# Performance work log

Measured on AMD Instinct MI355X. Metric: run time of the kernel, lower is better.

The kernel has to match this reference:

```python
import jax, jax.numpy as jnp
import numpy as np

B, S, D, H = 4, 1024, 1024, 16
HD = D // H  # head dim = 64


def setup_inputs() -> dict:
    key = jax.random.key(0)
    ks = jax.random.split(key, 12)
    inv = 1.0 / np.sqrt(D)
    inp = {
        "q": jax.random.normal(ks[0], (B, S, D), jnp.float32),
        "k": jax.random.normal(ks[1], (B, S, D), jnp.float32),
        "v": jax.random.normal(ks[2], (B, S, D), jnp.float32),
        # additive-style mask: 1 where attention is disallowed (causal)
        "mask": jnp.triu(jnp.ones((S, S), jnp.float32), k=1)[None, None, :, :],
        "Wq": jax.random.normal(ks[3], (D, D), jnp.float32) * inv,
        "bq": jnp.zeros((D,), jnp.float32),
        "Wk": jax.random.normal(ks[4], (D, D), jnp.float32) * inv,
        "bk": jnp.zeros((D,), jnp.float32),
        "Wv": jax.random.normal(ks[5], (D, D), jnp.float32) * inv,
        "bv": jnp.zeros((D,), jnp.float32),
        "Wo": jax.random.normal(ks[6], (D, D), jnp.float32) * inv,
        "bo": jnp.zeros((D,), jnp.float32),
    }
    return inp


def _split_heads(x):
    # [b, s, (h d)] -> [b, h, s, d]
    b, s, _ = x.shape
    return x.reshape(b, s, H, HD).transpose(0, 2, 1, 3)


def reference(q, k, v, mask, Wq, bq, Wk, bk, Wv, bv, Wo, bo):
    query = _split_heads(q @ Wq + bq)   # [b,h,s,d]
    key = _split_heads(k @ Wk + bk)
    value = _split_heads(v @ Wv + bv)

    scores = jnp.einsum("bhqd,bhkd->bhqk", query, key) / np.sqrt(HD)
    scores = scores + mask * (-1e12)
    attention_weights = jax.nn.softmax(scores, axis=-1)  # [b,h,s,s]
    attn = jnp.einsum("bhqk,bhkd->bhqd", attention_weights, value)

    # dropout is identity in eval mode
    attn = attn.transpose(0, 2, 1, 3).reshape(q.shape[0], q.shape[1], D)
    out = attn @ Wo + bo
    return out, attention_weights
```

## Files before the change

kernel.cpp:

```cpp
#include <hip/hip_runtime.h>
#include <hip/hip_bf16.h>

#define B_ 4
#define S_ 1024
#define D_ 1024
#define H_ 16
#define HD_ 64
#define M_ (B_*S_)
#define NT_ (S_/64)

typedef __attribute__((ext_vector_type(8))) short bf16x8;
typedef __attribute__((ext_vector_type(8))) unsigned short u16x8;
typedef __attribute__((ext_vector_type(4))) float f32x4;

typedef __attribute__((address_space(1))) const unsigned int g_uint;
typedef __attribute__((address_space(3))) unsigned int l_uint;

__device__ __forceinline__ unsigned short f2bf(float f) {
  unsigned int x = __builtin_bit_cast(unsigned int, f);
  unsigned int r = (x + 0x7fffu + ((x >> 16) & 1u)) >> 16;
  return (unsigned short)r;
}
__device__ __forceinline__ float bf2f(unsigned short u) {
  unsigned int x = ((unsigned int)u) << 16;
  return __builtin_bit_cast(float, x);
}
__device__ __forceinline__ void load_lds16(const ushort* g, ushort* l) {
  __builtin_amdgcn_global_load_lds((g_uint*)g, (l_uint*)l, 16, 0, 0);
}

__global__ void cvt3(const float* __restrict__ q, const float* __restrict__ k,
                     const float* __restrict__ v, ushort* __restrict__ qo,
                     ushort* __restrict__ ko, ushort* __restrict__ vo) {
  const float* s; ushort* d;
  switch (blockIdx.y) {
    case 0: s = q; d = qo; break;
    case 1: s = k; d = ko; break;
    default: s = v; d = vo; break;
  }
  int n4 = (M_ * D_) / 4;
  for (int i = blockIdx.x * blockDim.x + threadIdx.x; i < n4; i += gridDim.x * blockDim.x) {
    float4 x = reinterpret_cast<const float4*>(s)[i];
    ushort4 o;
    o.x = f2bf(x.x); o.y = f2bf(x.y); o.z = f2bf(x.z); o.w = f2bf(x.w);
    reinterpret_cast<ushort4*>(d)[i] = o;
  }
}

__global__ void tr4(const float* __restrict__ Wq, const float* __restrict__ Wk,
                    const float* __restrict__ Wv, const float* __restrict__ Wo,
                    ushort* __restrict__ q, ushort* __restrict__ k,
                    ushort* __restrict__ v, ushort* __restrict__ o) {
  const float* W; ushort* WT;
  switch (blockIdx.z) {
    case 0: W = Wq; WT = q; break;
    case 1: W = Wk; WT = k; break;
    case 2: W = Wv; WT = v; break;
    default: W = Wo; WT = o; break;
  }
  __shared__ float tile[32][33];
  int tx = threadIdx.x & 31, ty = threadIdx.x >> 5;
  int bx = blockIdx.x * 32, by = blockIdx.y * 32;
  for (int r = 0; r < 32; r += 8)
    tile[ty + r][tx] = W[(size_t)(by + ty + r) * D_ + bx + tx];
  __syncthreads();
  for (int r = 0; r < 32; r += 8)
    WT[(size_t)(bx + ty + r) * D_ + by + tx] = f2bf(tile[tx][ty + r]);
}

template <int BF16OUT>
__device__ __forceinline__ void gemm_body(const ushort* __restrict__ A,
                                          const ushort* __restrict__ Bt,
                                          const float* __restrict__ bias,
                                          void* __restrict__ Cp,
                                          int bm, int bn, int N, int K) {
  __shared__ ushort Al[128 * 64];
  __shared__ ushort Bl[64 * 64];
  const int tid = threadIdx.x;
  const int wave = tid >> 6, lane = tid & 63;
  const int r0 = lane & 15, kq = lane >> 4;
  const int wr = wave >> 1, wc = wave & 1;
  const int sl = lane >> 3;
  const int sc8 = ((lane & 7) ^ (lane >> 3)) * 8;
  f32x4 zero = {0.f, 0.f, 0.f, 0.f};
  f32x4 acc[4][2];
#pragma unroll
  for (int m = 0; m < 4; ++m)
    for (int n = 0; n < 2; ++n) acc[m][n] = zero;

  for (int kt = 0; kt < K; kt += 64) {
    __syncthreads();
#pragma unroll
    for (int i = 0; i < 6; ++i) {
      int c = wave * 6 + i;
      if (c < 16) {
        load_lds16(A + (size_t)(bm + c * 8 + sl) * K + kt + sc8, &Al[c * 512]);
      } else {
        int cb = c - 16;
        load_lds16(Bt + (size_t)(bn + cb * 8 + sl) * K + kt + sc8, &Bl[cb * 512]);
      }
    }
    __syncthreads();
#pragma unroll
    for (int kk = 0; kk < 2; ++kk) {
      bf16x8 a[4], b[2];
#pragma unroll
      for (int m = 0; m < 4; ++m) {
        int row = wr * 64 + m * 16 + r0;
        a[m] = *(const bf16x8*)&Al[row * 64 + (((kk * 4 + kq) ^ (r0 & 7)) * 8)];
      }
#pragma unroll
      for (int n = 0; n < 2; ++n) {
        int row = wc * 32 + n * 16 + r0;
        b[n] = *(const bf16x8*)&Bl[row * 64 + (((kk * 4 + kq) ^ (r0 & 7)) * 8)];
      }
#pragma unroll
      for (int m = 0; m < 4; ++m)
#pragma unroll
        for (int n = 0; n < 2; ++n)
          acc[m][n] = __builtin_amdgcn_mfma_f32_16x16x32_bf16(a[m], b[n], acc[m][n], 0, 0, 0);
    }
  }

#pragma unroll
  for (int m = 0; m < 4; ++m) {
#pragma unroll
    for (int n = 0; n < 2; ++n) {
      int col = bn + wc * 32 + n * 16 + r0;
      float bv = bias[col];
#pragma unroll
      for (int j = 0; j < 4; ++j) {
        int row = bm + wr * 64 + m * 16 + kq * 4 + j;
        float v = acc[m][n][j] + bv;
        if (BF16OUT) ((ushort*)Cp)[(size_t)row * N + col] = f2bf(v);
        else         ((float*)Cp)[(size_t)row * N + col] = v;
      }
    }
  }
}

__global__ __launch_bounds__(256) void gemm_qkv(const ushort* __restrict__ qa,
                                                const ushort* __restrict__ ka,
                                                const ushort* __restrict__ va,
                                                const ushort* __restrict__ WqT,
                                                const ushort* __restrict__ WkT,
                                                const ushort* __restrict__ WvT,
                                                const float* __restrict__ bq,
                                                const float* __restrict__ bk,
                                                const float* __restrict__ bv,
                                                ushort* __restrict__ Qo,
                                                ushort* __restrict__ Ko,
                                                ushort* __restrict__ Vo) {
  const ushort* A; const ushort* Bt; const float* bias; ushort* C;
  switch (blockIdx.z) {
    case 0: A = qa; Bt = WqT; bias = bq; C = Qo; break;
    case 1: A = ka; Bt = WkT; bias = bk; C = Ko; break;
    default: A = va; Bt = WvT; bias = bv; C = Vo; break;
  }
  gemm_body<1>(A, Bt, bias, C, blockIdx.x * 128, blockIdx.y * 64, D_, D_);
}

__global__ __launch_bounds__(256) void gemm_out(const ushort* __restrict__ A,
                                                const ushort* __restrict__ Bt,
                                                const float* __restrict__ bias,
                                                float* __restrict__ C) {
  gemm_body<0>(A, Bt, bias, C, blockIdx.x * 128, blockIdx.y * 64, D_, D_);
}

__global__ __launch_bounds__(256) void attn_fused(const ushort* __restrict__ Qb,
                                                  const ushort* __restrict__ Kb,
                                                  const ushort* __restrict__ Vb,
                                                  float* __restrict__ wout,
                                                  ushort* __restrict__ ctx) {
  const int h = blockIdx.y, b = blockIdx.z;
  const int tid = threadIdx.x, wave = tid >> 6, lane = tid & 63;
  const int r0 = lane & 15, kq = lane >> 4;
  const int sl = lane >> 3;
  const int sc8 = ((lane & 7) ^ (lane >> 3)) * 8;
  __shared__ ushort Qt[64 * 64];
  __shared__ ushort Kt[64 * 64];
  __shared__ ushort Vt[64 * 64];
  __shared__ ushort Wl[4][16 * 64];
  __shared__ float rs_lds[4][16];
  float* wbase = wout + (size_t)((b * H_ + h) * S_) * S_;

  for (int pp = 0; pp < 2; ++pp) {
    const int qt = pp ? (NT_ - 1 - blockIdx.x) : blockIdx.x;
    __syncthreads();
    {
      const ushort* Qg = Qb + ((size_t)(b * S_ + qt * 64)) * D_ + h * 64;
#pragma unroll
      for (int i = 0; i < 2; ++i) {
        int c = wave * 2 + i;
        load_lds16(Qg + (size_t)(c * 8 + sl) * D_ + sc8, &Qt[c * 512]);
      }
    }
    __syncthreads();
    bf16x8 qa0, qa1;
    {
      int row = wave * 16 + r0;
      qa0 = *(const bf16x8*)&Qt[row * 64 + ((kq ^ (r0 & 7)) * 8)];
      qa1 = *(const bf16x8*)&Qt[row * 64 + (((4 + kq) ^ (r0 & 7)) * 8)];
    }
    const int grow0 = qt * 64 + wave * 16 + kq * 4;

    float partial[4] = {0.f, 0.f, 0.f, 0.f};
    for (int vb = 0; vb <= qt; ++vb) {
      __syncthreads();
      const ushort* Kg = Kb + ((size_t)(b * S_ + vb * 64)) * D_ + h * 64;
#pragma unroll
      for (int i = 0; i < 2; ++i) {
        int c = wave * 2 + i;
        load_lds16(Kg + (size_t)(c * 8 + sl) * D_ + sc8, &Kt[c * 512]);
      }
      __syncthreads();
      const bool diag = (vb == qt);
#pragma unroll
      for (int jt = 0; jt < 4; ++jt) {
        int krow = jt * 16 + r0;
        bf16x8 kb0 = *(const bf16x8*)&Kt[krow * 64 + ((kq ^ (r0 & 7)) * 8)];
        bf16x8 kb1 = *(const bf16x8*)&Kt[krow * 64 + (((4 + kq) ^ (r0 & 7)) * 8)];
        f32x4 sc = {0.f, 0.f, 0.f, 0.f};
        sc = __builtin_amdgcn_mfma_f32_16x16x32_bf16(qa0, kb0, sc, 0, 0, 0);
        sc = __builtin_amdgcn_mfma_f32_16x16x32_bf16(qa1, kb1, sc, 0, 0, 0);
        int col = vb * 64 + krow;
#pragma unroll
        for (int j = 0; j < 4; ++j) {
          float e = (diag && col > grow0 + j) ? 0.f : __expf(sc[j] * 0.125f);
          partial[j] += e;
        }
      }
    }
    float rs[4];
#pragma unroll
    for (int j = 0; j < 4; ++j) {
      float s = partial[j];
#pragma unroll
      for (int off = 1; off < 16; off <<= 1) s += __shfl_xor(s, off, 64);
      rs[j] = 1.f / s;
    }
    if (r0 == 0) {
#pragma unroll
      for (int j = 0; j < 4; ++j) rs_lds[wave][kq * 4 + j] = rs[j];
    }

    f32x4 zero = {0.f, 0.f, 0.f, 0.f};
    f32x4 cacc[4];
#pragma unroll
    for (int nt = 0; nt < 4; ++nt) cacc[nt] = zero;

    for (int vb = 0; vb <= qt; ++vb) {
      __syncthreads();
      const ushort* Kg = Kb + ((size_t)(b * S_ + vb * 64)) * D_ + h * 64;
      const ushort* Vg = Vb + ((size_t)(b * S_ + vb * 64)) * D_ + h * 64;
#pragma unroll
      for (int i = 0; i < 2; ++i) {
        int c = wave * 2 + i;
        load_lds16(Kg + (size_t)(c * 8 + sl) * D_ + sc8, &Kt[c * 512]);
      }
#pragma unroll
      for (int it = 0; it < 2; ++it) {
        int seg = wave * 2 + it;
        ushort tmp[8];
        *(uint4*)tmp = *(const uint4*)&Vg[(size_t)lane * D_ + seg * 8];
#pragma unroll
        for (int e = 0; e < 8; ++e) Vt[(seg * 8 + e) * 64 + (lane ^ (e << 3))] = tmp[e];
      }
      __syncthreads();
      const bool diag = (vb == qt);
#pragma unroll
      for (int jt = 0; jt < 4; ++jt) {
        int krow = jt * 16 + r0;
        bf16x8 kb0 = *(const bf16x8*)&Kt[krow * 64 + ((kq ^ (r0 & 7)) * 8)];
        bf16x8 kb1 = *(const bf16x8*)&Kt[krow * 64 + (((4 + kq) ^ (r0 & 7)) * 8)];
        f32x4 sc = {0.f, 0.f, 0.f, 0.f};
        sc = __builtin_amdgcn_mfma_f32_16x16x32_bf16(qa0, kb0, sc, 0, 0, 0);
        sc = __builtin_amdgcn_mfma_f32_16x16x32_bf16(qa1, kb1, sc, 0, 0, 0);
        int col = vb * 64 + krow;
#pragma unroll
        for (int j = 0; j < 4; ++j) {
          int rowW = kq * 4 + j;
          float e = (diag && col > grow0 + j) ? 0.f : __expf(sc[j] * 0.125f);
          Wl[wave][rowW * 64 + ((jt * 16 + r0) ^ ((rowW & 7) << 3))] = f2bf(e);
        }
      }
#pragma unroll
      for (int ks = 0; ks < 2; ++ks) {
        bf16x8 af = *(const bf16x8*)&Wl[wave][r0 * 64 + (((ks * 4 + kq) ^ (r0 & 7)) * 8)];
#pragma unroll
        for (int nt = 0; nt < 4; ++nt) {
          bf16x8 vf = *(const bf16x8*)&Vt[(nt * 16 + r0) * 64 + (((ks * 4 + kq) ^ (r0 & 7)) * 8)];
          cacc[nt] = __builtin_amdgcn_mfma_f32_16x16x32_bf16(af, vf, cacc[nt], 0, 0, 0);
        }
      }
      {
        int row16 = lane >> 2, c4 = lane & 3;
        float scl = rs_lds[wave][row16];
        int slotA = (2 * c4) ^ (row16 & 7);
        int slotB = (2 * c4 + 1) ^ (row16 & 7);
        u16x8 w0 = *(const u16x8*)&Wl[wave][row16 * 64 + slotA * 8];
        u16x8 w1 = *(const u16x8*)&Wl[wave][row16 * 64 + slotB * 8];
        float* dst = &wbase[(size_t)(qt * 64 + wave * 16 + row16) * S_ + vb * 64 + c4 * 16];
        f32x4 o0 = {bf2f(w0[0]) * scl, bf2f(w0[1]) * scl, bf2f(w0[2]) * scl, bf2f(w0[3]) * scl};
        f32x4 o1 = {bf2f(w0[4]) * scl, bf2f(w0[5]) * scl, bf2f(w0[6]) * scl, bf2f(w0[7]) * scl};
        f32x4 o2 = {bf2f(w1[0]) * scl, bf2f(w1[1]) * scl, bf2f(w1[2]) * scl, bf2f(w1[3]) * scl};
        f32x4 o3 = {bf2f(w1[4]) * scl, bf2f(w1[5]) * scl, bf2f(w1[6]) * scl, bf2f(w1[7]) * scl};
        *(f32x4*)&dst[0]  = o0;
        *(f32x4*)&dst[4]  = o1;
        *(f32x4*)&dst[8]  = o2;
        *(f32x4*)&dst[12] = o3;
      }
    }

    {
      int col0 = (qt + 1) * 64;
      int nf4 = (S_ - col0) >> 2;
      int row = tid >> 2, c = tid & 3;
      f32x4 z4 = {0.f, 0.f, 0.f, 0.f};
      float* rp = &wbase[(size_t)(qt * 64 + row) * S_];
      for (int i = c; i < nf4; i += 4) *(f32x4*)&rp[col0 + i * 4] = z4;
    }

    {
      ushort* cg = ctx + ((size_t)(b * S_ + qt * 64 + wave * 16 + kq * 4)) * D_ + h * 64;
#pragma unroll
      for (int nt = 0; nt < 4; ++nt)
#pragma unroll
        for (int j = 0; j < 4; ++j)
          cg[(size_t)j * D_ + nt * 16 + r0] = f2bf(cacc[nt][j] * rs[j]);
    }
  }
}

extern "C" void kernel_launch(void* const* d_in, const int* in_sizes, int n_in,
                              void* d_out, int out_size, void* d_ws, size_t ws_size,
                              hipStream_t stream) {
  const float* q    = (const float*)d_in[0];
  const float* k    = (const float*)d_in[1];
  const float* v    = (const float*)d_in[2];
  const float* Wq   = (const float*)d_in[4];
  const float* bq   = (const float*)d_in[5];
  const float* Wk   = (const float*)d_in[6];
  const float* bk   = (const float*)d_in[7];
  const float* Wv   = (const float*)d_in[8];
  const float* bv   = (const float*)d_in[9];
  const float* Wo   = (const float*)d_in[10];
  const float* bo   = (const float*)d_in[11];

  char* ws = (char*)d_ws;
  const size_t MB = 1024 * 1024;
  ushort* q_bf   = (ushort*)(ws + 0 * MB);
  ushort* k_bf   = (ushort*)(ws + 8 * MB);
  ushort* v_bf   = (ushort*)(ws + 16 * MB);
  ushort* WqT    = (ushort*)(ws + 24 * MB);
  ushort* WkT    = (ushort*)(ws + 26 * MB);
  ushort* WvT    = (ushort*)(ws + 28 * MB);
  ushort* WoT    = (ushort*)(ws + 30 * MB);
  ushort* Q_bf   = (ushort*)(ws + 32 * MB);
  ushort* K_bf   = (ushort*)(ws + 40 * MB);
  ushort* V_bf   = (ushort*)(ws + 48 * MB);
  ushort* ctx_bf = (ushort*)(ws + 56 * MB);

  float* out  = (float*)d_out;
  float* wout = out + (size_t)M_ * D_;

  cvt3<<<dim3(2048, 3), 256, 0, stream>>>(q, k, v, q_bf, k_bf, v_bf);
  tr4<<<dim3(32, 32, 4), 256, 0, stream>>>(Wq, Wk, Wv, Wo, WqT, WkT, WvT, WoT);
  gemm_qkv<<<dim3(M_ / 128, D_ / 64, 3), 256, 0, stream>>>(
      q_bf, k_bf, v_bf, WqT, WkT, WvT, bq, bk, bv, Q_bf, K_bf, V_bf);
  attn_fused<<<dim3(NT_ / 2, H_, B_), 256, 0, stream>>>(Q_bf, K_bf, V_bf, wout, ctx_bf);
  gemm_out<<<dim3(M_ / 128, D_ / 64), 256, 0, stream>>>(ctx_bf, WoT, bo, out);
}
```

Measured before the change: 186.0 us.

## Enlarge GEMM tiles to 128x128 and double-buffer K/V staging in attention

The GEMM tiles grow from 128x64 to 128x128, so each wave computes a 64x64 sub-tile and A-tile reuse improves, at the cost of more accumulator registers and fewer blocks. The attention kernel double-buffers K (and V, through registers) so the next block's global loads overlap with the current MFMA work. Q fragments are now read directly from global memory into registers instead of through LDS. Blocks are remapped to a flat 1D grid that interleaves heads and batches. The change raises LDS use and register pressure, which can lower occupancy.

```diff
diff --git a/kernel.cpp b/kernel.cpp
--- a/kernel.cpp
+++ b/kernel.cpp
@@ -75,49 +75,42 @@
                                           void* __restrict__ Cp,
                                           int bm, int bn, int N, int K) {
   __shared__ ushort Al[128 * 64];
-  __shared__ ushort Bl[64 * 64];
+  __shared__ ushort Bl[128 * 64];
   const int tid = threadIdx.x;
   const int wave = tid >> 6, lane = tid & 63;
   const int r0 = lane & 15, kq = lane >> 4;
   const int wr = wave >> 1, wc = wave & 1;
   const int sl = lane >> 3;
-  const int sc8 = ((lane & 7) ^ (lane >> 3)) * 8;
+  const int sc8 = ((lane & 7) ^ sl) * 8;
   f32x4 zero = {0.f, 0.f, 0.f, 0.f};
-  f32x4 acc[4][2];
+  f32x4 acc[4][4];
 #pragma unroll
   for (int m = 0; m < 4; ++m)
-    for (int n = 0; n < 2; ++n) acc[m][n] = zero;
+#pragma unroll
+    for (int n = 0; n < 4; ++n) acc[m][n] = zero;
 
   for (int kt = 0; kt < K; kt += 64) {
     __syncthreads();
 #pragma unroll
-    for (int i = 0; i < 6; ++i) {
-      int c = wave * 6 + i;
-      if (c < 16) {
-        load_lds16(A + (size_t)(bm + c * 8 + sl) * K + kt + sc8, &Al[c * 512]);
-      } else {
-        int cb = c - 16;
-        load_lds16(Bt + (size_t)(bn + cb * 8 + sl) * K + kt + sc8, &Bl[cb * 512]);
-      }
+    for (int i = 0; i < 4; ++i) {
+      int c = wave * 4 + i;
+      load_lds16(A  + (size_t)(bm + c * 8 + sl) * K + kt + sc8, &Al[c * 512]);
+      load_lds16(Bt + (size_t)(bn + c * 8 + sl) * K + kt + sc8, &Bl[c * 512]);
     }
     __syncthreads();
 #pragma unroll
     for (int kk = 0; kk < 2; ++kk) {
-      bf16x8 a[4], b[2];
-#pragma unroll
-      for (int m = 0; m < 4; ++m) {
-        int row = wr * 64 + m * 16 + r0;
-        a[m] = *(const bf16x8*)&Al[row * 64 + (((kk * 4 + kq) ^ (r0 & 7)) * 8)];
-      }
-#pragma unroll
-      for (int n = 0; n < 2; ++n) {
-        int row = wc * 32 + n * 16 + r0;
-        b[n] = *(const bf16x8*)&Bl[row * 64 + (((kk * 4 + kq) ^ (r0 & 7)) * 8)];
-      }
+      bf16x8 a[4], b[4];
 #pragma unroll
       for (int m = 0; m < 4; ++m)
-#pragma unroll
-        for (int n = 0; n < 2; ++n)
+        a[m] = *(const bf16x8*)&Al[(wr * 64 + m * 16 + r0) * 64 + (((kk * 4 + kq) ^ (r0 & 7)) * 8)];
+#pragma unroll
+      for (int n = 0; n < 4; ++n)
+        b[n] = *(const bf16x8*)&Bl[(wc * 64 + n * 16 + r0) * 64 + (((kk * 4 + kq) ^ (r0 & 7)) * 8)];
+#pragma unroll
+      for (int m = 0; m < 4; ++m)
+#pragma unroll
+        for (int n = 0; n < 4; ++n)
           acc[m][n] = __builtin_amdgcn_mfma_f32_16x16x32_bf16(a[m], b[n], acc[m][n], 0, 0, 0);
     }
   }
@@ -125,8 +118,8 @@
 #pragma unroll
   for (int m = 0; m < 4; ++m) {
 #pragma unroll
-    for (int n = 0; n < 2; ++n) {
-      int col = bn + wc * 32 + n * 16 + r0;
+    for (int n = 0; n < 4; ++n) {
+      int col = bn + wc * 64 + n * 16 + r0;
       float bv = bias[col];
 #pragma unroll
       for (int j = 0; j < 4; ++j) {
@@ -157,14 +150,14 @@
     case 1: A = ka; Bt = WkT; bias = bk; C = Ko; break;
     default: A = va; Bt = WvT; bias = bv; C = Vo; break;
   }
-  gemm_body<1>(A, Bt, bias, C, blockIdx.x * 128, blockIdx.y * 64, D_, D_);
+  gemm_body<1>(A, Bt, bias, C, blockIdx.x * 128, blockIdx.y * 128, D_, D_);
 }
 
 __global__ __launch_bounds__(256) void gemm_out(const ushort* __restrict__ A,
                                                 const ushort* __restrict__ Bt,
                                                 const float* __restrict__ bias,
                                                 float* __restrict__ C) {
-  gemm_body<0>(A, Bt, bias, C, blockIdx.x * 128, blockIdx.y * 64, D_, D_);
+  gemm_body<0>(A, Bt, bias, C, blockIdx.x * 128, blockIdx.y * 128, D_, D_);
 }
 
 __global__ __launch_bounds__(256) void attn_fused(const ushort* __restrict__ Qb,
@@ -172,54 +165,52 @@
                                                   const ushort* __restrict__ Vb,
                                                   float* __restrict__ wout,
                                                   ushort* __restrict__ ctx) {
-  const int h = blockIdx.y, b = blockIdx.z;
+  const int id = blockIdx.x;
+  const int h = (id & 7) | (((id >> 3) & 1) << 3);
+  const int b = (id >> 4) & 3;
+  const int px = id >> 6;
   const int tid = threadIdx.x, wave = tid >> 6, lane = tid & 63;
   const int r0 = lane & 15, kq = lane >> 4;
   const int sl = lane >> 3;
-  const int sc8 = ((lane & 7) ^ (lane >> 3)) * 8;
-  __shared__ ushort Qt[64 * 64];
-  __shared__ ushort Kt[64 * 64];
-  __shared__ ushort Vt[64 * 64];
+  const int sc8 = ((lane & 7) ^ sl) * 8;
+  __shared__ ushort Kt[2][64 * 64];
+  __shared__ ushort Vt[2][64 * 64];
   __shared__ ushort Wl[4][16 * 64];
   __shared__ float rs_lds[4][16];
   float* wbase = wout + (size_t)((b * H_ + h) * S_) * S_;
+  const size_t bh_off = ((size_t)(b * S_)) * D_ + (size_t)h * 64;
 
   for (int pp = 0; pp < 2; ++pp) {
-    const int qt = pp ? (NT_ - 1 - blockIdx.x) : blockIdx.x;
+    const int qt = pp ? (NT_ - 1 - px) : px;
     __syncthreads();
-    {
-      const ushort* Qg = Qb + ((size_t)(b * S_ + qt * 64)) * D_ + h * 64;
+
+    const ushort* Qg = Qb + bh_off + (size_t)(qt * 64 + wave * 16 + r0) * D_ + kq * 8;
+    bf16x8 qa0 = *(const bf16x8*)Qg;
+    bf16x8 qa1 = *(const bf16x8*)(Qg + 32);
+    const int grow0 = qt * 64 + wave * 16 + kq * 4;
+
+    auto stage_K = [&](int buf, int vb) {
+      const ushort* Kg = Kb + bh_off + (size_t)(vb * 64) * D_;
 #pragma unroll
       for (int i = 0; i < 2; ++i) {
         int c = wave * 2 + i;
-        load_lds16(Qg + (size_t)(c * 8 + sl) * D_ + sc8, &Qt[c * 512]);
-      }
-    }
-    __syncthreads();
-    bf16x8 qa0, qa1;
-    {
-      int row = wave * 16 + r0;
-      qa0 = *(const bf16x8*)&Qt[row * 64 + ((kq ^ (r0 & 7)) * 8)];
-      qa1 = *(const bf16x8*)&Qt[row * 64 + (((4 + kq) ^ (r0 & 7)) * 8)];
-    }
-    const int grow0 = qt * 64 + wave * 16 + kq * 4;
-
+        load_lds16(Kg + (size_t)(c * 8 + sl) * D_ + sc8, &Kt[buf][c * 512]);
+      }
+    };
+
+    int cur = 0;
+    stage_K(0, 0);
     float partial[4] = {0.f, 0.f, 0.f, 0.f};
     for (int vb = 0; vb <= qt; ++vb) {
-      __syncthreads();
-      const ushort* Kg = Kb + ((size_t)(b * S_ + vb * 64)) * D_ + h * 64;
-#pragma unroll
-      for (int i = 0; i < 2; ++i) {
-        int c = wave * 2 + i;
-        load_lds16(Kg + (size_t)(c * 8 + sl) * D_ + sc8, &Kt[c * 512]);
-      }
-      __syncthreads();
+      asm volatile("s_waitcnt vmcnt(0)" ::: "memory");
+      __builtin_amdgcn_s_barrier();
+      if (vb < qt) stage_K(cur ^ 1, vb + 1);
       const bool diag = (vb == qt);
 #pragma unroll
       for (int jt = 0; jt < 4; ++jt) {
         int krow = jt * 16 + r0;
-        bf16x8 kb0 = *(const bf16x8*)&Kt[krow * 64 + ((kq ^ (r0 & 7)) * 8)];
-        bf16x8 kb1 = *(const bf16x8*)&Kt[krow * 64 + (((4 + kq) ^ (r0 & 7)) * 8)];
+        bf16x8 kb0 = *(const bf16x8*)&Kt[cur][krow * 64 + ((kq ^ (r0 & 7)) * 8)];
+        bf16x8 kb1 = *(const bf16x8*)&Kt[cur][krow * 64 + (((4 + kq) ^ (r0 & 7)) * 8)];
         f32x4 sc = {0.f, 0.f, 0.f, 0.f};
         sc = __builtin_amdgcn_mfma_f32_16x16x32_bf16(qa0, kb0, sc, 0, 0, 0);
         sc = __builtin_amdgcn_mfma_f32_16x16x32_bf16(qa1, kb1, sc, 0, 0, 0);
@@ -230,6 +221,7 @@
           partial[j] += e;
         }
       }
+      cur ^= 1;
     }
     float rs[4];
 #pragma unroll
@@ -249,30 +241,37 @@
 #pragma unroll
     for (int nt = 0; nt < 4; ++nt) cacc[nt] = zero;
 
-    for (int vb = 0; vb <= qt; ++vb) {
-      __syncthreads();
-      const ushort* Kg = Kb + ((size_t)(b * S_ + vb * 64)) * D_ + h * 64;
-      const ushort* Vg = Vb + ((size_t)(b * S_ + vb * 64)) * D_ + h * 64;
-#pragma unroll
-      for (int i = 0; i < 2; ++i) {
-        int c = wave * 2 + i;
-        load_lds16(Kg + (size_t)(c * 8 + sl) * D_ + sc8, &Kt[c * 512]);
-      }
+    __syncthreads();
+    uint4 vr[2];
+    auto vload = [&](int vb) {
+      const ushort* Vg = Vb + bh_off + (size_t)(vb * 64) * D_;
+      vr[0] = *(const uint4*)&Vg[(size_t)lane * D_ + (size_t)(wave * 2 + 0) * 8];
+      vr[1] = *(const uint4*)&Vg[(size_t)lane * D_ + (size_t)(wave * 2 + 1) * 8];
+    };
+    auto vwrite = [&](int buf) {
 #pragma unroll
       for (int it = 0; it < 2; ++it) {
         int seg = wave * 2 + it;
         ushort tmp[8];
-        *(uint4*)tmp = *(const uint4*)&Vg[(size_t)lane * D_ + seg * 8];
-#pragma unroll
-        for (int e = 0; e < 8; ++e) Vt[(seg * 8 + e) * 64 + (lane ^ (e << 3))] = tmp[e];
-      }
-      __syncthreads();
+        *(uint4*)tmp = vr[it];
+#pragma unroll
+        for (int e = 0; e < 8; ++e) Vt[buf][(seg * 8 + e) * 64 + (lane ^ (e << 3))] = tmp[e];
+      }
+    };
+    cur = 0;
+    stage_K(0, 0);
+    vload(0);
+    vwrite(0);
+    for (int vb = 0; vb <= qt; ++vb) {
+      asm volatile("s_waitcnt vmcnt(0) lgkmcnt(0)" ::: "memory");
+      __builtin_amdgcn_s_barrier();
+      if (vb < qt) { stage_K(cur ^ 1, vb + 1); vload(vb + 1); }
       const bool diag = (vb == qt);
 #pragma unroll
       for (int jt = 0; jt < 4; ++jt) {
         int krow = jt * 16 + r0;
-        bf16x8 kb0 = *(const bf16x8*)&Kt[krow * 64 + ((kq ^ (r0 & 7)) * 8)];
-        bf16x8 kb1 = *(const bf16x8*)&Kt[krow * 64 + (((4 + kq) ^ (r0 & 7)) * 8)];
+        bf16x8 kb0 = *(const bf16x8*)&Kt[cur][krow * 64 + ((kq ^ (r0 & 7)) * 8)];
+        bf16x8 kb1 = *(const bf16x8*)&Kt[cur][krow * 64 + (((4 + kq) ^ (r0 & 7)) * 8)];
         f32x4 sc = {0.f, 0.f, 0.f, 0.f};
         sc = __builtin_amdgcn_mfma_f32_16x16x32_bf16(qa0, kb0, sc, 0, 0, 0);
         sc = __builtin_amdgcn_mfma_f32_16x16x32_bf16(qa1, kb1, sc, 0, 0, 0);
@@ -289,7 +288,7 @@
         bf16x8 af = *(const bf16x8*)&Wl[wave][r0 * 64 + (((ks * 4 + kq) ^ (r0 & 7)) * 8)];
 #pragma unroll
         for (int nt = 0; nt < 4; ++nt) {
-          bf16x8 vf = *(const bf16x8*)&Vt[(nt * 16 + r0) * 64 + (((ks * 4 + kq) ^ (r0 & 7)) * 8)];
+          bf16x8 vf = *(const bf16x8*)&Vt[cur][(nt * 16 + r0) * 64 + (((ks * 4 + kq) ^ (r0 & 7)) * 8)];
           cacc[nt] = __builtin_amdgcn_mfma_f32_16x16x32_bf16(af, vf, cacc[nt], 0, 0, 0);
         }
       }
@@ -310,6 +309,8 @@
         *(f32x4*)&dst[8]  = o2;
         *(f32x4*)&dst[12] = o3;
       }
+      if (vb < qt) vwrite(cur ^ 1);
+      cur ^= 1;
     }
 
     {
@@ -366,8 +367,8 @@
 
   cvt3<<<dim3(2048, 3), 256, 0, stream>>>(q, k, v, q_bf, k_bf, v_bf);
   tr4<<<dim3(32, 32, 4), 256, 0, stream>>>(Wq, Wk, Wv, Wo, WqT, WkT, WvT, WoT);
-  gemm_qkv<<<dim3(M_ / 128, D_ / 64, 3), 256, 0, stream>>>(
+  gemm_qkv<<<dim3(M_ / 128, D_ / 128, 3), 256, 0, stream>>>(
       q_bf, k_bf, v_bf, WqT, WkT, WvT, bq, bk, bv, Q_bf, K_bf, V_bf);
-  attn_fused<<<dim3(NT_ / 2, H_, B_), 256, 0, stream>>>(Q_bf, K_bf, V_bf, wout, ctx_bf);
-  gemm_out<<<dim3(M_ / 128, D_ / 64), 256, 0, stream>>>(ctx_bf, WoT, bo, out);
-}
+  attn_fused<<<dim3(512), 256, 0, stream>>>(Q_bf, K_bf, V_bf, wout, ctx_bf);
+  gemm_out<<<dim3(M_ / 128, D_ / 128), 256, 0, stream>>>(ctx_bf, WoT, bo, out);
+}
```

New measurement: 175.7 us. -5.5%, faster.
